# Kernel tuning notes

Measured on AMD Instinct MI355X. Metric: run time of the kernel, lower is better.

Reference implementation:

```python
import jax, jax.numpy as jnp
import numpy as np

ALPHA, GAMMA = 0.25, 2.0
POS_T, NEG_T = 0.5, 0.4
SCALE = jnp.array([0.1, 0.1, 0.2, 0.2], dtype=jnp.float32)
B, A, C, M = 8, 120000, 80, 32


def setup_inputs() -> dict:
    key = jax.random.key(0)
    k1, k2, k3, k4, k5, k6 = jax.random.split(key, 6)
    classifications = jax.random.uniform(k1, (B, A, C), dtype=jnp.float32)
    regressions = jax.random.normal(k2, (B, A, 4), dtype=jnp.float32)
    # anchors: centers in [0,640), sizes in [16,256) -> (x1,y1,x2,y2)
    ctr = jax.random.uniform(k3, (A, 2), dtype=jnp.float32) * 640.0
    wh = jax.random.uniform(k4, (A, 2), dtype=jnp.float32) * 240.0 + 16.0
    anchors = jnp.concatenate([ctr - 0.5 * wh, ctr + 0.5 * wh], axis=1)[None]
    # labels: [B, M, 5] = (x1, y1, x2, y2, class); last 8 boxes padded (-1)
    xy1 = jax.random.uniform(k5, (B, M, 2), dtype=jnp.float32) * 512.0
    bwh = jax.random.uniform(k6, (B, M, 2), dtype=jnp.float32) * 120.0 + 8.0
    cls = jax.random.randint(jax.random.fold_in(key, 7), (B, M), 0, C).astype(jnp.float32)
    cls = jnp.where(jnp.arange(M)[None, :] >= M - 8, -1.0, cls)
    labels = jnp.concatenate([xy1, xy1 + bwh, cls[..., None]], axis=2)
    return {"classifications": classifications, "regressions": regressions,
            "anchors": anchors, "labels": labels}


def _calc_iou(a, b):
    # a: [A,4] anchors, b: [M,4] gt boxes -> [A,M]
    area_b = (b[:, 2] - b[:, 0]) * (b[:, 3] - b[:, 1])
    iw = jnp.clip(jnp.minimum(a[:, 2:3], b[None, :, 2]) - jnp.maximum(a[:, 0:1], b[None, :, 0]), 0)
    ih = jnp.clip(jnp.minimum(a[:, 3:4], b[None, :, 3]) - jnp.maximum(a[:, 1:2], b[None, :, 1]), 0)
    area_a = ((a[:, 2] - a[:, 0]) * (a[:, 3] - a[:, 1]))[:, None]
    inter = iw * ih
    ua = jnp.clip(area_a + area_b[None, :] - inter, 1e-8)
    return inter / ua


def _focal_fwd(classifications, regressions, anchors, labels):
    anchor = anchors[0]                      # [A,4]
    aw = anchor[:, 2] - anchor[:, 0]
    ah = anchor[:, 3] - anchor[:, 1]
    acx = anchor[:, 0] + 0.5 * aw
    acy = anchor[:, 1] + 0.5 * ah

    def per_image(cls_p, reg, lab):
        cls_p = jnp.clip(cls_p, 1e-4, 1.0 - 1e-4)          # [A,C]
        valid = lab[:, 4] != -1.0                          # [M]
        iou = _calc_iou(anchor, lab[:, :4])                # [A,M]
        iou = jnp.where(valid[None, :], iou, -1.0)
        iou_max = iou.max(axis=1)
        iou_arg = iou.argmax(axis=1)
        pos = iou_max >= POS_T                             # [A]
        neg = iou_max < NEG_T
        assigned = lab[iou_arg]                            # [A,5]
        onehot = jax.nn.one_hot(assigned[:, 4].astype(jnp.int32), C, dtype=cls_p.dtype)
        targets = jnp.where(pos[:, None], onehot,
                            jnp.where(neg[:, None], 0.0, -1.0))
        is_one = targets == 1.0
        alpha_f = jnp.where(is_one, ALPHA, 1.0 - ALPHA)
        focal_w = alpha_f * jnp.where(is_one, 1.0 - cls_p, cls_p) ** GAMMA
        bce = -(targets * jnp.log(cls_p) + (1.0 - targets) * jnp.log(1.0 - cls_p))
        cls_loss = jnp.where(targets != -1.0, focal_w * bce, 0.0).sum()
        num_pos = pos.sum().astype(cls_p.dtype)
        c_loss = cls_loss / jnp.maximum(num_pos, 1.0)
        gw_raw = assigned[:, 2] - assigned[:, 0]
        gh_raw = assigned[:, 3] - assigned[:, 1]
        gcx = assigned[:, 0] + 0.5 * gw_raw
        gcy = assigned[:, 1] + 0.5 * gh_raw
        gw = jnp.clip(gw_raw, 1.0)
        gh = jnp.clip(gh_raw, 1.0)
        t = jnp.stack([(gcx - acx) / aw, (gcy - acy) / ah,
                       jnp.log(gw / aw), jnp.log(gh / ah)], axis=1) / SCALE
        diff = jnp.abs(t - reg)
        sl1 = jnp.where(diff <= 1.0 / 9.0, 0.5 * 9.0 * diff ** 2, diff - 0.5 / 9.0)
        r_sum = jnp.where(pos[:, None], sl1, 0.0).sum()
        r_loss = jnp.where(num_pos > 0, r_sum / jnp.maximum(num_pos * 4.0, 1.0), 0.0)
        return c_loss, r_loss

    c_losses, r_losses = jax.vmap(per_image)(classifications, regressions, labels)
    return c_losses.mean(), r_losses.mean()


def reference(classifications, regressions, anchors, labels):
    return _focal_fwd(classifications, regressions, anchors, labels)
```

## Files before the change

### kernel.cpp

```cpp
#include <hip/hip_runtime.h>

#define BB 8
#define AA 120000
#define CC 80
#define MM 32

constexpr float ALPHA_ = 0.25f;
constexpr float POS_T_ = 0.5f;
constexpr float NEG_T_ = 0.4f;


__global__ void init_acc_kernel(float* __restrict__ acc) {
    int t = threadIdx.x;
    if (t < 24) acc[t] = 0.0f;
}

__global__ void assign_kernel(const float* __restrict__ anchors,
                              const float* __restrict__ regressions,
                              const float* __restrict__ labels,
                              float* __restrict__ acc,
                              unsigned short* __restrict__ status) {
    const int b = blockIdx.y;
    const int a = blockIdx.x * blockDim.x + threadIdx.x;

    __shared__ float lb[MM * 5];
    __shared__ float blk_r, blk_n;
    if (threadIdx.x < MM * 5) lb[threadIdx.x] = labels[b * MM * 5 + threadIdx.x];
    if (threadIdx.x == 0) { blk_r = 0.0f; blk_n = 0.0f; }
    __syncthreads();

    float r_contrib = 0.0f, n_contrib = 0.0f;

    if (a < AA) {
        const float4 an = ((const float4*)anchors)[a];
        const float aw = an.z - an.x;
        const float ah = an.w - an.y;
        const float area_a = aw * ah;

        float best = -1e30f;
        int arg = 0;
        #pragma unroll 8
        for (int m = 0; m < MM; ++m) {
            const float bx1 = lb[m * 5 + 0], by1 = lb[m * 5 + 1];
            const float bx2 = lb[m * 5 + 2], by2 = lb[m * 5 + 3];
            float v;
            if (lb[m * 5 + 4] == -1.0f) {
                v = -1.0f;
            } else {
                float iw = fminf(an.z, bx2) - fmaxf(an.x, bx1);
                iw = fmaxf(iw, 0.0f);
                float ih = fminf(an.w, by2) - fmaxf(an.y, by1);
                ih = fmaxf(ih, 0.0f);
                const float inter = iw * ih;
                const float ua = fmaxf(area_a + (bx2 - bx1) * (by2 - by1) - inter, 1e-8f);
                v = inter / ua;
            }
            if (v > best) { best = v; arg = m; }
        }

        const bool pos = best >= POS_T_;
        const bool neg = best < NEG_T_;
        const int acls = (int)lb[arg * 5 + 4];
        unsigned short st = pos ? (unsigned short)(2 | (acls << 2)) : (neg ? 0 : 1);
        status[(size_t)b * AA + a] = st;

        if (pos) {
            n_contrib = 1.0f;
            const float gx1 = lb[arg * 5 + 0], gy1 = lb[arg * 5 + 1];
            const float gx2 = lb[arg * 5 + 2], gy2 = lb[arg * 5 + 3];
            const float gwr = gx2 - gx1, ghr = gy2 - gy1;
            const float gcx = gx1 + 0.5f * gwr, gcy = gy1 + 0.5f * ghr;
            const float gw = fmaxf(gwr, 1.0f), gh = fmaxf(ghr, 1.0f);
            const float acx = an.x + 0.5f * aw, acy = an.y + 0.5f * ah;

            const float t0 = ((gcx - acx) / aw) / 0.1f;
            const float t1 = ((gcy - acy) / ah) / 0.1f;
            const float t2 = logf(gw / aw) / 0.2f;
            const float t3 = logf(gh / ah) / 0.2f;

            const float4 rg = ((const float4*)regressions)[(size_t)b * AA + a];
            const float d0 = fabsf(t0 - rg.x);
            const float d1 = fabsf(t1 - rg.y);
            const float d2 = fabsf(t2 - rg.z);
            const float d3 = fabsf(t3 - rg.w);
            const float bnd = 1.0f / 9.0f;
            const float hb  = 0.5f / 9.0f;
            r_contrib  = (d0 <= bnd) ? 4.5f * d0 * d0 : d0 - hb;
            r_contrib += (d1 <= bnd) ? 4.5f * d1 * d1 : d1 - hb;
            r_contrib += (d2 <= bnd) ? 4.5f * d2 * d2 : d2 - hb;
            r_contrib += (d3 <= bnd) ? 4.5f * d3 * d3 : d3 - hb;
        }
    }

    #pragma unroll
    for (int off = 32; off > 0; off >>= 1) {
        r_contrib += __shfl_down(r_contrib, off);
        n_contrib += __shfl_down(n_contrib, off);
    }
    if ((threadIdx.x & 63) == 0) {
        atomicAdd(&blk_r, r_contrib);
        atomicAdd(&blk_n, n_contrib);
    }
    __syncthreads();
    if (threadIdx.x == 0) {
        if (blk_r != 0.0f) atomicAdd(&acc[8 + b], blk_r);
        if (blk_n != 0.0f) atomicAdd(&acc[16 + b], blk_n);
    }
}

#define IPT 8
#define F4_PER_IMG (AA * CC / 4)

__global__ __launch_bounds__(256) void cls_loss_kernel(
        const float* __restrict__ cls,
        const unsigned short* __restrict__ status,
        float* __restrict__ acc) {
    const int b = blockIdx.y;
    const float4* __restrict__ cp = (const float4*)(cls + (size_t)b * AA * CC);
    const unsigned short* __restrict__ stp = status + (size_t)b * AA;

    float sum = 0.0f;
    const int base = blockIdx.x * (256 * IPT) + threadIdx.x;

    #pragma unroll
    for (int i = 0; i < IPT; ++i) {
        const int j = base + i * 256;
        if (j < F4_PER_IMG) {
            const int a = j / 20;
            const unsigned short st = stp[a];
            const int s = st & 3;
            if (s != 1) {
                const float4 p4 = cp[j];
                const int cbase = (j % 20) * 4;
                const int acls = (s == 2) ? (int)(st >> 2) : -1;
                const float pv[4] = {p4.x, p4.y, p4.z, p4.w};
                #pragma unroll
                for (int k = 0; k < 4; ++k) {
                    const float p = fminf(fmaxf(pv[k], 1e-4f), 1.0f - 1e-4f);
                    if (cbase + k == acls) {
                        const float q = 1.0f - p;
                        sum += ALPHA_ * q * q * (-__logf(p));
                    } else {
                        sum += (1.0f - ALPHA_) * p * p * (-__logf(1.0f - p));
                    }
                }
            }
        }
    }

    #pragma unroll
    for (int off = 32; off > 0; off >>= 1) sum += __shfl_down(sum, off);
    __shared__ float wsum[4];
    const int wid = threadIdx.x >> 6;
    if ((threadIdx.x & 63) == 0) wsum[wid] = sum;
    __syncthreads();
    if (threadIdx.x == 0) {
        atomicAdd(&acc[b], wsum[0] + wsum[1] + wsum[2] + wsum[3]);
    }
}

__global__ void finalize_kernel(const float* __restrict__ acc, float* __restrict__ out) {
    if (threadIdx.x == 0 && blockIdx.x == 0) {
        float cm = 0.0f, rm = 0.0f;
        #pragma unroll
        for (int b = 0; b < BB; ++b) {
            const float np_ = acc[16 + b];
            cm += acc[b] / fmaxf(np_, 1.0f);
            rm += (np_ > 0.0f) ? acc[8 + b] / (np_ * 4.0f) : 0.0f;
        }
        out[0] = cm / (float)BB;
        out[1] = rm / (float)BB;
    }
}

extern "C" void kernel_launch(void* const* d_in, const int* in_sizes, int n_in,
                              void* d_out, int out_size, void* d_ws, size_t ws_size,
                              hipStream_t stream) {
    const float* classifications = (const float*)d_in[0];
    const float* regressions     = (const float*)d_in[1];
    const float* anchors         = (const float*)d_in[2];
    const float* labels          = (const float*)d_in[3];
    float* out = (float*)d_out;

    float* acc = (float*)d_ws;
    unsigned short* status = (unsigned short*)((char*)d_ws + 128);

    init_acc_kernel<<<1, 32, 0, stream>>>(acc);

    dim3 g1((AA + 255) / 256, BB);
    assign_kernel<<<g1, 256, 0, stream>>>(anchors, regressions, labels, acc, status);

    dim3 g2((F4_PER_IMG + 256 * IPT - 1) / (256 * IPT), BB);
    cls_loss_kernel<<<g2, 256, 0, stream>>>(classifications, status, acc);

    finalize_kernel<<<1, 64, 0, stream>>>(acc, out);
}
```

Measured before the change: 505.5 us.

## Fuse anchor assignment and classification loss into one kernel via shared status

The anchor-assignment and classification-loss kernels are merged into one. Each block handles 192 anchors: it computes their status into shared memory and then streams the matching slice of classification probabilities. This drops the global status buffer round-trip and one kernel launch. In exchange, 64 of the 256 threads sit idle during assignment, and the IoU phase now runs serially before the bandwidth-bound loads in each block.

```diff
diff --git a/kernel.cpp b/kernel.cpp
--- a/kernel.cpp
+++ b/kernel.cpp
@@ -4,6 +4,10 @@
 #define AA 120000
 #define CC 80
 #define MM 32
+
+#define APB 192
+#define F4B (APB * 20)
+#define NBLK (AA / APB)
 
 constexpr float ALPHA_ = 0.25f;
 constexpr float POS_T_ = 0.5f;
@@ -15,23 +19,26 @@
     if (t < 24) acc[t] = 0.0f;
 }
 
-__global__ void assign_kernel(const float* __restrict__ anchors,
-                              const float* __restrict__ regressions,
-                              const float* __restrict__ labels,
-                              float* __restrict__ acc,
-                              unsigned short* __restrict__ status) {
-    const int b = blockIdx.y;
-    const int a = blockIdx.x * blockDim.x + threadIdx.x;
+__global__ __launch_bounds__(256) void fused_kernel(
+        const float* __restrict__ anchors,
+        const float* __restrict__ cls,
+        const float* __restrict__ regressions,
+        const float* __restrict__ labels,
+        float* __restrict__ acc) {
+    const int b  = blockIdx.y;
+    const int a0 = blockIdx.x * APB;
+    const int t  = threadIdx.x;
 
     __shared__ float lb[MM * 5];
-    __shared__ float blk_r, blk_n;
-    if (threadIdx.x < MM * 5) lb[threadIdx.x] = labels[b * MM * 5 + threadIdx.x];
-    if (threadIdx.x == 0) { blk_r = 0.0f; blk_n = 0.0f; }
+    __shared__ unsigned short sst[APB];
+    __shared__ float wred[2][4];
+
+    if (t < MM * 5) lb[t] = labels[b * MM * 5 + t];
     __syncthreads();
 
-    float r_contrib = 0.0f, n_contrib = 0.0f;
-
-    if (a < AA) {
+    float r_c = 0.0f, n_c = 0.0f;
+    if (t < APB) {
+        const int a = a0 + t;
         const float4 an = ((const float4*)anchors)[a];
         const float aw = an.z - an.x;
         const float ah = an.w - an.y;
@@ -47,10 +54,8 @@
             if (lb[m * 5 + 4] == -1.0f) {
                 v = -1.0f;
             } else {
-                float iw = fminf(an.z, bx2) - fmaxf(an.x, bx1);
-                iw = fmaxf(iw, 0.0f);
-                float ih = fminf(an.w, by2) - fmaxf(an.y, by1);
-                ih = fmaxf(ih, 0.0f);
+                float iw = fmaxf(fminf(an.z, bx2) - fmaxf(an.x, bx1), 0.0f);
+                float ih = fmaxf(fminf(an.w, by2) - fmaxf(an.y, by1), 0.0f);
                 const float inter = iw * ih;
                 const float ua = fmaxf(area_a + (bx2 - bx1) * (by2 - by1) - inter, 1e-8f);
                 v = inter / ua;
@@ -61,11 +66,10 @@
         const bool pos = best >= POS_T_;
         const bool neg = best < NEG_T_;
         const int acls = (int)lb[arg * 5 + 4];
-        unsigned short st = pos ? (unsigned short)(2 | (acls << 2)) : (neg ? 0 : 1);
-        status[(size_t)b * AA + a] = st;
+        sst[t] = pos ? (unsigned short)(2 | (acls << 2)) : (neg ? (unsigned short)0 : (unsigned short)1);
 
         if (pos) {
-            n_contrib = 1.0f;
+            n_c = 1.0f;
             const float gx1 = lb[arg * 5 + 0], gy1 = lb[arg * 5 + 1];
             const float gx2 = lb[arg * 5 + 2], gy2 = lb[arg * 5 + 3];
             const float gwr = gx2 - gx1, ghr = gy2 - gy1;
@@ -73,10 +77,10 @@
             const float gw = fmaxf(gwr, 1.0f), gh = fmaxf(ghr, 1.0f);
             const float acx = an.x + 0.5f * aw, acy = an.y + 0.5f * ah;
 
-            const float t0 = ((gcx - acx) / aw) / 0.1f;
-            const float t1 = ((gcy - acy) / ah) / 0.1f;
-            const float t2 = logf(gw / aw) / 0.2f;
-            const float t3 = logf(gh / ah) / 0.2f;
+            const float t0 = ((gcx - acx) / aw) * 10.0f;
+            const float t1 = ((gcy - acy) / ah) * 10.0f;
+            const float t2 = logf(gw / aw) * 5.0f;
+            const float t3 = logf(gh / ah) * 5.0f;
 
             const float4 rg = ((const float4*)regressions)[(size_t)b * AA + a];
             const float d0 = fabsf(t0 - rg.x);
@@ -85,64 +89,51 @@
             const float d3 = fabsf(t3 - rg.w);
             const float bnd = 1.0f / 9.0f;
             const float hb  = 0.5f / 9.0f;
-            r_contrib  = (d0 <= bnd) ? 4.5f * d0 * d0 : d0 - hb;
-            r_contrib += (d1 <= bnd) ? 4.5f * d1 * d1 : d1 - hb;
-            r_contrib += (d2 <= bnd) ? 4.5f * d2 * d2 : d2 - hb;
-            r_contrib += (d3 <= bnd) ? 4.5f * d3 * d3 : d3 - hb;
+            r_c  = (d0 <= bnd) ? 4.5f * d0 * d0 : d0 - hb;
+            r_c += (d1 <= bnd) ? 4.5f * d1 * d1 : d1 - hb;
+            r_c += (d2 <= bnd) ? 4.5f * d2 * d2 : d2 - hb;
+            r_c += (d3 <= bnd) ? 4.5f * d3 * d3 : d3 - hb;
         }
     }
 
     #pragma unroll
     for (int off = 32; off > 0; off >>= 1) {
-        r_contrib += __shfl_down(r_contrib, off);
-        n_contrib += __shfl_down(n_contrib, off);
+        r_c += __shfl_down(r_c, off);
+        n_c += __shfl_down(n_c, off);
     }
-    if ((threadIdx.x & 63) == 0) {
-        atomicAdd(&blk_r, r_contrib);
-        atomicAdd(&blk_n, n_contrib);
+    const int wid = t >> 6;
+    if ((t & 63) == 0) { wred[0][wid] = r_c; wred[1][wid] = n_c; }
+    __syncthreads();
+    if (t == 0) {
+        const float rs = wred[0][0] + wred[0][1] + wred[0][2] + wred[0][3];
+        const float ns = wred[1][0] + wred[1][1] + wred[1][2] + wred[1][3];
+        if (rs != 0.0f) atomicAdd(&acc[8 + b], rs);
+        if (ns != 0.0f) atomicAdd(&acc[16 + b], ns);
     }
-    __syncthreads();
-    if (threadIdx.x == 0) {
-        if (blk_r != 0.0f) atomicAdd(&acc[8 + b], blk_r);
-        if (blk_n != 0.0f) atomicAdd(&acc[16 + b], blk_n);
-    }
-}
 
-#define IPT 8
-#define F4_PER_IMG (AA * CC / 4)
-
-__global__ __launch_bounds__(256) void cls_loss_kernel(
-        const float* __restrict__ cls,
-        const unsigned short* __restrict__ status,
-        float* __restrict__ acc) {
-    const int b = blockIdx.y;
-    const float4* __restrict__ cp = (const float4*)(cls + (size_t)b * AA * CC);
-    const unsigned short* __restrict__ stp = status + (size_t)b * AA;
+    const float4* __restrict__ cp =
+        (const float4*)(cls + (size_t)b * AA * CC) + (size_t)a0 * 20;
 
     float sum = 0.0f;
-    const int base = blockIdx.x * (256 * IPT) + threadIdx.x;
-
     #pragma unroll
-    for (int i = 0; i < IPT; ++i) {
-        const int j = base + i * 256;
-        if (j < F4_PER_IMG) {
-            const int a = j / 20;
-            const unsigned short st = stp[a];
-            const int s = st & 3;
-            if (s != 1) {
-                const float4 p4 = cp[j];
-                const int cbase = (j % 20) * 4;
-                const int acls = (s == 2) ? (int)(st >> 2) : -1;
-                const float pv[4] = {p4.x, p4.y, p4.z, p4.w};
-                #pragma unroll
-                for (int k = 0; k < 4; ++k) {
-                    const float p = fminf(fmaxf(pv[k], 1e-4f), 1.0f - 1e-4f);
-                    if (cbase + k == acls) {
-                        const float q = 1.0f - p;
-                        sum += ALPHA_ * q * q * (-__logf(p));
-                    } else {
-                        sum += (1.0f - ALPHA_) * p * p * (-__logf(1.0f - p));
-                    }
+    for (int i = 0; i < F4B / 256; ++i) {
+        const int j = i * 256 + t;
+        const int a = j / 20;
+        const unsigned short st = sst[a];
+        const int s = st & 3;
+        if (s != 1) {
+            const float4 p4 = cp[j];
+            const int cbase = (j - a * 20) * 4;
+            const int acls = (s == 2) ? (int)(st >> 2) : -1;
+            const float pv[4] = {p4.x, p4.y, p4.z, p4.w};
+            #pragma unroll
+            for (int k = 0; k < 4; ++k) {
+                const float p = fminf(fmaxf(pv[k], 1e-4f), 1.0f - 1e-4f);
+                if (cbase + k == acls) {
+                    const float q = 1.0f - p;
+                    sum += ALPHA_ * q * q * (-__logf(p));
+                } else {
+                    sum += (1.0f - ALPHA_) * p * p * (-__logf(1.0f - p));
                 }
             }
         }
@@ -150,12 +141,11 @@
 
     #pragma unroll
     for (int off = 32; off > 0; off >>= 1) sum += __shfl_down(sum, off);
-    __shared__ float wsum[4];
-    const int wid = threadIdx.x >> 6;
-    if ((threadIdx.x & 63) == 0) wsum[wid] = sum;
     __syncthreads();
-    if (threadIdx.x == 0) {
-        atomicAdd(&acc[b], wsum[0] + wsum[1] + wsum[2] + wsum[3]);
+    if ((t & 63) == 0) wred[0][wid] = sum;
+    __syncthreads();
+    if (t == 0) {
+        atomicAdd(&acc[b], wred[0][0] + wred[0][1] + wred[0][2] + wred[0][3]);
     }
 }
 
@@ -181,17 +171,12 @@
     const float* anchors         = (const float*)d_in[2];
     const float* labels          = (const float*)d_in[3];
     float* out = (float*)d_out;
-
     float* acc = (float*)d_ws;
-    unsigned short* status = (unsigned short*)((char*)d_ws + 128);
 
     init_acc_kernel<<<1, 32, 0, stream>>>(acc);
 
-    dim3 g1((AA + 255) / 256, BB);
-    assign_kernel<<<g1, 256, 0, stream>>>(anchors, regressions, labels, acc, status);
-
-    dim3 g2((F4_PER_IMG + 256 * IPT - 1) / (256 * IPT), BB);
-    cls_loss_kernel<<<g2, 256, 0, stream>>>(classifications, status, acc);
+    dim3 g(NBLK, BB);
+    fused_kernel<<<g, 256, 0, stream>>>(anchors, classifications, regressions, labels, acc);
 
     finalize_kernel<<<1, 64, 0, stream>>>(acc, out);
 }
```

Result: faster. 465.8 us (-7.9%).
